# Performance work log

Measured on AMD Instinct MI355X. Metric: run time of the kernel, lower is better.

## Reference

```python
import math
import jax, jax.numpy as jnp
import numpy as np


def _gelu(x):
    return jax.nn.gelu(x, approximate=False)


def _bilinear_sample(feat, gx, gy):
    """grid_sample, mode=bilinear, padding=border, align_corners=True.
    feat: [B,C,H,W]; gx,gy: [B,M] in [-1,1]. Returns [B,M,C]."""
    B, C, H, W = feat.shape
    x = jnp.clip((gx + 1.0) * 0.5 * (W - 1), 0.0, W - 1)
    y = jnp.clip((gy + 1.0) * 0.5 * (H - 1), 0.0, H - 1)
    x0 = jnp.floor(x); y0 = jnp.floor(y)
    wx = (x - x0)[..., None]; wy = (y - y0)[..., None]
    x0i = x0.astype(jnp.int32); y0i = y0.astype(jnp.int32)
    x1i = jnp.minimum(x0i + 1, W - 1); y1i = jnp.minimum(y0i + 1, H - 1)
    ft = jnp.transpose(feat, (0, 2, 3, 1))  # [B,H,W,C]
    gather = jax.vmap(lambda f, yi, xi: f[yi, xi])
    v00 = gather(ft, y0i, x0i); v01 = gather(ft, y0i, x1i)
    v10 = gather(ft, y1i, x0i); v11 = gather(ft, y1i, x1i)
    return (v00 * (1 - wx) * (1 - wy) + v01 * wx * (1 - wy)
            + v10 * (1 - wx) * wy + v11 * wx * wy)


def _layernorm(x, w, b, eps=1e-5):
    m = jnp.mean(x, -1, keepdims=True)
    v = jnp.var(x, -1, keepdims=True)
    return (x - m) / jnp.sqrt(v + eps) * w + b


def _gfb(h, f_next, ph_w, ph_b, gate, w1, b1, w2, b2, ln_w, ln_b):
    g = jax.nn.sigmoid(gate)
    fused = f_next + g * (h @ ph_w + ph_b)
    fused = _gelu(fused @ w1 + b1) @ w2 + b2
    return _layernorm(fused, ln_w, ln_b)


def _forward(img, feat_s8, feat_s16, coarse_flow, query_coords,
             pp_w1, pp_b1, pp_w2, pp_b2, p8_w, p8_b, p16_w, p16_b,
             f1_ph_w, f1_ph_b, f1_gate, f1_w1, f1_b1, f1_w2, f1_b2, f1_ln_w, f1_ln_b,
             f2_ph_w, f2_ph_b, f2_gate, f2_w1, f2_b1, f2_w2, f2_b2, f2_ln_w, f2_ln_b,
             h_w1, h_b1, h_w2, h_b2, h_w3, h_b3):
    B, _, H, W = img.shape
    N = query_coords.shape[1]
    k = 5; half = k // 2
    H8, W8 = coarse_flow.shape[2], coarse_flow.shape[3]
    # normalized grid at query points (x,y)
    gx = 2.0 * query_coords[..., 0] / (W - 1) - 1.0
    gy = 2.0 * query_coords[..., 1] / (H - 1) - 1.0
    coarse_q = _bilinear_sample(coarse_flow, gx, gy)  # [B,N,2]
    coarse_q = coarse_q * jnp.array([W / W8, H / H8], coarse_q.dtype)
    # local k x k RGB patches
    offs = jnp.arange(-half, half + 1, dtype=img.dtype)
    oy, ox = jnp.meshgrid(offs, offs, indexing='ij')
    og = jnp.stack([ox.reshape(-1), oy.reshape(-1)], -1)  # [k*k,2]
    ce = query_coords[:, :, None, :] + og                # [B,N,kk,2]
    pgx = (2.0 * ce[..., 0] / (W - 1) - 1.0).reshape(B, -1)
    pgy = (2.0 * ce[..., 1] / (H - 1) - 1.0).reshape(B, -1)
    patches = _bilinear_sample(img, pgx, pgy).reshape(B, N, k * k * 3)
    f_local = _gelu(patches @ pp_w1 + pp_b1) @ pp_w2 + pp_b2
    f8 = _bilinear_sample(feat_s8, gx, gy) @ p8_w + p8_b
    f16 = _bilinear_sample(feat_s16, gx, gy) @ p16_w + p16_b
    D = f_local.shape[-1]
    h = f_local.reshape(B * N, D)
    h = _gfb(h, f8.reshape(B * N, D), f1_ph_w, f1_ph_b, f1_gate,
             f1_w1, f1_b1, f1_w2, f1_b2, f1_ln_w, f1_ln_b)
    h = _gfb(h, f16.reshape(B * N, D), f2_ph_w, f2_ph_b, f2_gate,
             f2_w1, f2_b1, f2_w2, f2_b2, f2_ln_w, f2_ln_b)
    # relative-in-cell coords + sinusoidal PE (6 bands)
    qx = query_coords[..., 0] / (W / W8)
    qy = query_coords[..., 1] / (H / H8)
    local = jnp.stack([(qx - jnp.round(qx)) * 2.0, (qy - jnp.round(qy)) * 2.0], -1)
    freqs = (2.0 ** jnp.arange(6, dtype=local.dtype)) * math.pi
    xf = local[..., None] * freqs                        # [B,N,2,6]
    enc = jnp.concatenate([jnp.sin(xf), jnp.cos(xf)], -1).reshape(B, N, 24)
    pe = jnp.concatenate([local, enc], -1).reshape(B * N, 26)
    coarse_flat = coarse_q.reshape(B * N, 2)
    mi = jnp.concatenate([h, pe, coarse_flat], -1)       # [B*N, 156]
    delta = _gelu(_gelu(mi @ h_w1 + h_b1) @ h_w2 + h_b2) @ h_w3 + h_b3
    return (coarse_flat + delta).reshape(B, N, 2)


def setup_inputs() -> dict:
    key = jax.random.key(0)
    ks = jax.random.split(key, 40)
    B, H, W = 2, 384, 512
    H8, W8, H16, W16 = 48, 64, 24, 32
    N, D, k = 65536, 128, 5
    pf = 3 * k * k
    def p(i, shape):
        return jax.random.normal(ks[i], shape, jnp.float32) * 0.05
    return {
        'img': jax.random.uniform(ks[0], (B, 3, H, W), jnp.float32),
        'feat_s8': jax.random.normal(ks[1], (B, D, H8, W8), jnp.float32),
        'feat_s16': jax.random.normal(ks[2], (B, D, H16, W16), jnp.float32),
        'coarse_flow': jax.random.normal(ks[3], (B, 2, H8, W8), jnp.float32),
        'query_coords': jax.random.uniform(ks[4], (B, N, 2), jnp.float32)
                        * jnp.array([W - 1.0, H - 1.0], jnp.float32),
        'pp_w1': p(5, (pf, D)), 'pp_b1': p(6, (D,)),
        'pp_w2': p(7, (D, D)), 'pp_b2': p(8, (D,)),
        'p8_w': p(9, (D, D)), 'p8_b': p(10, (D,)),
        'p16_w': p(11, (D, D)), 'p16_b': p(12, (D,)),
        'f1_ph_w': p(13, (D, D)), 'f1_ph_b': p(14, (D,)), 'f1_gate': p(15, (D,)),
        'f1_w1': p(16, (D, 2 * D)), 'f1_b1': p(17, (2 * D,)),
        'f1_w2': p(18, (2 * D, D)), 'f1_b2': p(19, (D,)),
        'f1_ln_w': 1.0 + p(20, (D,)), 'f1_ln_b': p(21, (D,)),
        'f2_ph_w': p(22, (D, D)), 'f2_ph_b': p(23, (D,)), 'f2_gate': p(24, (D,)),
        'f2_w1': p(25, (D, 2 * D)), 'f2_b1': p(26, (2 * D,)),
        'f2_w2': p(27, (2 * D, D)), 'f2_b2': p(28, (D,)),
        'f2_ln_w': 1.0 + p(29, (D,)), 'f2_ln_b': p(30, (D,)),
        'h_w1': p(31, (D + 26 + 2, 128)), 'h_b1': p(32, (128,)),
        'h_w2': p(33, (128, 64)), 'h_b2': p(34, (64,)),
        'h_w3': p(35, (64, 2)), 'h_b3': p(36, (2,)),
    }


def reference(img, feat_s8, feat_s16, coarse_flow, query_coords,
              pp_w1, pp_b1, pp_w2, pp_b2, p8_w, p8_b, p16_w, p16_b,
              f1_ph_w, f1_ph_b, f1_gate, f1_w1, f1_b1, f1_w2, f1_b2, f1_ln_w, f1_ln_b,
              f2_ph_w, f2_ph_b, f2_gate, f2_w1, f2_b1, f2_w2, f2_b2, f2_ln_w, f2_ln_b,
              h_w1, h_b1, h_w2, h_b2, h_w3, h_b3):
    return _forward(img, feat_s8, feat_s16, coarse_flow, query_coords,
                    pp_w1, pp_b1, pp_w2, pp_b2, p8_w, p8_b, p16_w, p16_b,
                    f1_ph_w, f1_ph_b, f1_gate, f1_w1, f1_b1, f1_w2, f1_b2, f1_ln_w, f1_ln_b,
                    f2_ph_w, f2_ph_b, f2_gate, f2_w1, f2_b1, f2_w2, f2_b2, f2_ln_w, f2_ln_b,
                    h_w1, h_b1, h_w2, h_b2, h_w3, h_b3)
```

## Files before the change

kernel.cpp:

```cpp
#include <hip/hip_runtime.h>
#include <math.h>

#define NT 512
#define MB 64
#define MTOT 131072
#define IMG_H 384
#define IMG_W 512
#define H8 48
#define W8 64
#define H16 24
#define W16 32

#define SAB 128
#define SPE 40

typedef _Float16 half8_t __attribute__((ext_vector_type(8)));
typedef _Float16 half4_t __attribute__((ext_vector_type(4)));
typedef float f32x4_t __attribute__((ext_vector_type(4)));
typedef unsigned short u16;

#define SWZ(r, gi) ((gi) ^ ((r) & 7))

#define PW_PP1    0
#define PW_MEGA1  12288
#define PW_S8     77824
#define PW_MEGA2  110592
#define PW_S15    176128
#define PW_HW1    208896
#define PW_HW2    229376
#define PW_END    237568
#define FT8_OFF   PW_END
#define FT8_CNT   (2*H8*W8*128)
#define FT16_OFF  (FT8_OFF + FT8_CNT)
#define FT16_CNT  (2*H16*W16*128)
#define F32_OFF   (FT16_OFF + FT16_CNT)
#define PEG_OFF   (F32_OFF + 2*164480)
#define PEG_CNT   (2048*MB*SPE)
#define CBG_OFF   (PEG_OFF + PEG_CNT)

__device__ __forceinline__ u16 tohalf(float v) {
  return __builtin_bit_cast(u16, (_Float16)v);
}
__device__ __forceinline__ float geluf(float x) {
  float x2 = x * x;
  float t = x * fmaf(x2, 0.0713548162726f, 1.5957691216057308f);
  float e = __expf(-t);
  return x * __builtin_amdgcn_rcpf(1.0f + e);
}

__device__ __forceinline__ float bilin_plane(const float* __restrict__ plane,
                                             int Wd, int Hd, float x, float y) {
  x = fminf(fmaxf(x, 0.f), (float)(Wd - 1));
  y = fminf(fmaxf(y, 0.f), (float)(Hd - 1));
  float x0f = floorf(x), y0f = floorf(y);
  int x0 = (int)x0f, y0 = (int)y0f;
  int x1 = min(x0 + 1, Wd - 1), y1 = min(y0 + 1, Hd - 1);
  float wx = x - x0f, wy = y - y0f;
  const float* r0 = plane + y0 * Wd;
  const float* r1 = plane + y1 * Wd;
  float v00 = r0[x0], v01 = r0[x1], v10 = r1[x0], v11 = r1[x1];
  float top = v00 + wx * (v01 - v00);
  float bot = v10 + wx * (v11 - v10);
  return top + wy * (bot - top);
}

__device__ __forceinline__ void featSample(const u16* __restrict__ ft, int Wd, int Hd,
                                           float x, float y, u16* dstRow,
                                           int i16, int giS) {
  x = fminf(fmaxf(x, 0.f), (float)(Wd - 1));
  y = fminf(fmaxf(y, 0.f), (float)(Hd - 1));
  float x0f = floorf(x), y0f = floorf(y);
  int x0 = (int)x0f, y0 = (int)y0f;
  int x1 = min(x0 + 1, Wd - 1), y1 = min(y0 + 1, Hd - 1);
  _Float16 wx = (_Float16)(x - x0f), wy = (_Float16)(y - y0f);
  half8_t v00 = *reinterpret_cast<const half8_t*>(ft + (y0 * Wd + x0) * 128 + i16 * 8);
  half8_t v01 = *reinterpret_cast<const half8_t*>(ft + (y0 * Wd + x1) * 128 + i16 * 8);
  half8_t v10 = *reinterpret_cast<const half8_t*>(ft + (y1 * Wd + x0) * 128 + i16 * 8);
  half8_t v11 = *reinterpret_cast<const half8_t*>(ft + (y1 * Wd + x1) * 128 + i16 * 8);
  half8_t top = v00 + wx * (v01 - v00);
  half8_t bot = v10 + wx * (v11 - v10);
  half8_t r = top + wy * (bot - top);
  *reinterpret_cast<half8_t*>(dstRow + giS * 8) = r;
}

template <int KT, int SPLITKT, int ACT, int SWB = 1, int NWAVES = 8>
__device__ __forceinline__ void mmv(
    const u16* __restrict__ wpk,
    const u16* aA, const u16* aB, int strB,
    const float* __restrict__ bias,
    u16* ob) {
  const int tid = threadIdx.x;
  const int lane = tid & 63;
  const int w = tid >> 6;
  const int l15 = lane & 15;
  const int g = lane >> 4;
  if (NWAVES == 8 || w < NWAVES) {
    f32x4_t acc[4];
#pragma unroll
    for (int mt = 0; mt < 4; ++mt) acc[mt] = (f32x4_t){0.f, 0.f, 0.f, 0.f};
    __builtin_amdgcn_s_setprio(1);
#pragma unroll
    for (int kt = 0; kt < KT; ++kt) {
      half8_t af[4];
#pragma unroll
      for (int mt = 0; mt < 4; ++mt) {
        const int row = mt * 16 + l15;
        const u16* p;
        if (kt < SPLITKT) {
          p = aA + row * 128 + SWZ(row, kt * 4 + g) * 8;
        } else if (SWB) {
          p = aB + row * 128 + SWZ(row, (kt - SPLITKT) * 4 + g) * 8;
        } else {
          p = aB + row * strB + (kt - SPLITKT) * 32 + g * 8;
        }
        af[mt] = *reinterpret_cast<const half8_t*>(p);
      }
      half8_t bf = *reinterpret_cast<const half8_t*>(wpk + ((w * KT + kt) * 64 + lane) * 8);
#pragma unroll
      for (int mt = 0; mt < 4; ++mt)
        acc[mt] = __builtin_amdgcn_mfma_f32_16x16x32_f16(bf, af[mt], acc[mt], 0, 0, 0);
    }
    __builtin_amdgcn_s_setprio(0);
    const int c0 = (w << 4) + (g << 2);
    f32x4_t bv = *reinterpret_cast<const f32x4_t*>(bias + c0);
#pragma unroll
    for (int mt = 0; mt < 4; ++mt) {
      const int row = (mt << 4) + l15;
      half4_t hv;
#pragma unroll
      for (int r = 0; r < 4; ++r) {
        float v = acc[mt][r] + bv[r];
        if (ACT == 1) v = geluf(v);
        hv[r] = (_Float16)v;
      }
      const int e = row * 128 + (c0 ^ ((row & 7) << 3));
      *reinterpret_cast<half4_t*>(ob + e) = hv;
    }
  }
}

__device__ __forceinline__ void lnorm(const u16* src, u16* dst,
                                      const float* __restrict__ lw,
                                      const float* __restrict__ lb) {
  const int tid = threadIdx.x;
  int q = tid >> 3, s = tid & 7;
  float xs[16];
  float sum = 0.f, sum2 = 0.f;
#pragma unroll
  for (int c8 = 0; c8 < 2; ++c8) {
    const int gi = SWZ(q, 2 * s + c8);
    half8_t v = *reinterpret_cast<const half8_t*>(src + q * 128 + gi * 8);
#pragma unroll
    for (int j = 0; j < 8; ++j) {
      float x = (float)v[j];
      xs[c8 * 8 + j] = x; sum += x; sum2 += x * x;
    }
  }
  sum += __shfl_xor(sum, 1); sum2 += __shfl_xor(sum2, 1);
  sum += __shfl_xor(sum, 2); sum2 += __shfl_xor(sum2, 2);
  sum += __shfl_xor(sum, 4); sum2 += __shfl_xor(sum2, 4);
  float mean = sum * 0.0078125f;
  float var = sum2 * 0.0078125f - mean * mean;
  float rstd = rsqrtf(var + 1e-5f);
#pragma unroll
  for (int c8 = 0; c8 < 2; ++c8) {
    half8_t r;
#pragma unroll
    for (int j = 0; j < 8; ++j) {
      int c = s * 16 + c8 * 8 + j;
      r[j] = (_Float16)((xs[c8 * 8 + j] - mean) * rstd * lw[c] + lb[c]);
    }
    const int gi = SWZ(q, 2 * s + c8);
    *reinterpret_cast<half8_t*>(dst + q * 128 + gi * 8) = r;
  }
}

__global__ void compose1(const float* __restrict__ pp_w2, const float* __restrict__ f1_ph_w,
                         const float* __restrict__ f1_gate, const float* __restrict__ f2_ph_w,
                         const float* __restrict__ f2_gate, const float* __restrict__ p8_b,
                         const float* __restrict__ f1_ph_b, const float* __restrict__ pp_b2,
                         float* __restrict__ Wbot1, float* __restrict__ Wph2s,
                         float* __restrict__ bf1) {
  int idx = blockIdx.x * blockDim.x + threadIdx.x;
  if (idx >= 16384) return;
  int k = idx >> 7, m = idx & 127;
  float sig1 = 1.f / (1.f + expf(-f1_gate[m]));
  float acc = 0.f;
  for (int r = 0; r < 128; ++r) acc += pp_w2[k * 128 + r] * f1_ph_w[r * 128 + m];
  Wbot1[idx] = acc * sig1;
  Wph2s[idx] = f2_ph_w[idx] * (1.f / (1.f + expf(-f2_gate[m])));
  if (k == 0) {
    float b = 0.f;
    for (int r = 0; r < 128; ++r) b += pp_b2[r] * f1_ph_w[r * 128 + m];
    bf1[m] = p8_b[m] + sig1 * f1_ph_b[m] + sig1 * b;
  }
}

__global__ void composeW(const float* __restrict__ p8_w, const float* __restrict__ Wbot1,
                         const float* __restrict__ f1_w1, const float* __restrict__ p16_w,
                         const float* __restrict__ Wph2s, const float* __restrict__ f2_w1,
                         const float* __restrict__ bf1, const float* __restrict__ f1_b1,
                         const float* __restrict__ p16_b, const float* __restrict__ f2_ph_b,
                         const float* __restrict__ f2_gate, const float* __restrict__ f2_b1,
                         float* __restrict__ WAf, float* __restrict__ WBf,
                         float* __restrict__ bA, float* __restrict__ bB) {
  const int n = threadIdx.x;
  const int kb = blockIdx.x;
  if (kb < 256) {
    const float* A = (kb < 128) ? (p8_w + kb * 128) : (Wbot1 + (kb - 128) * 128);
    float acc = 0.f;
    for (int m = 0; m < 128; ++m) acc += A[m] * f1_w1[m * 256 + n];
    WAf[kb * 256 + n] = acc;
  } else if (kb < 512) {
    const int k = kb - 256;
    const float* A = (k < 128) ? (p16_w + k * 128) : (Wph2s + (k - 128) * 128);
    float acc = 0.f;
    for (int m = 0; m < 128; ++m) acc += A[m] * f2_w1[m * 256 + n];
    WBf[k * 256 + n] = acc;
  } else if (kb == 512) {
    float acc = f1_b1[n];
    for (int m = 0; m < 128; ++m) acc += bf1[m] * f1_w1[m * 256 + n];
    bA[n] = acc;
  } else {
    float acc = f2_b1[n];
    for (int m = 0; m < 128; ++m) {
      float sig2 = 1.f / (1.f + expf(-f2_gate[m]));
      acc += (p16_b[m] + sig2 * f2_ph_b[m]) * f2_w1[m * 256 + n];
    }
    bB[n] = acc;
  }
}

struct PackArgs {
  const float *pp_w1, *f1_w2, *f2_w2, *h_w1, *h_w2;
  const float *WAf, *WBf;
  u16* dst;
};

__global__ void pack_weights(PackArgs a) {
  const int KTs[7]   = {3, 8, 8, 8, 8, 5, 4};
  const int Ks[7]    = {75, 256, 256, 256, 256, 156, 128};
  const int bases[8] = {0, 12288, 77824, 110592, 176128, 208896, 229376, 237568};
  int stride = gridDim.x * blockDim.x;
  for (int i = blockIdx.x * blockDim.x + threadIdx.x; i < PW_END; i += stride) {
    int s = 0;
    while (i >= bases[s + 1]) ++s;
    int rem = i - bases[s];
    int e = rem & 511, lane = e >> 3, j = e & 7;
    int ntkt = rem >> 9;
    int kt = ntkt % KTs[s], nt = ntkt / KTs[s];
    int k = kt * 32 + ((lane >> 4) << 3) + j;
    int col = (nt << 4) + (lane & 15);
    float v = 0.f;
    if (k < Ks[s]) {
      switch (s) {
        case 0: v = a.pp_w1[k * 128 + col]; break;
        case 1: v = a.WAf[k * 256 + col]; break;
        case 2: v = a.f1_w2[k * 128 + col]; break;
        case 3: v = a.WBf[k * 256 + col]; break;
        case 4: v = a.f2_w2[k * 128 + col]; break;
        case 5: v = a.h_w1[k * 128 + col]; break;
        case 6: v = a.h_w2[k * 64 + col]; break;
      }
    }
    a.dst[i] = tohalf(v);
  }
}

__global__ void cvt_cl_all(const float* __restrict__ s8, u16* __restrict__ d8,
                           const float* __restrict__ s16, u16* __restrict__ d16) {
  const int tot8 = 2 * 128 * H8 * W8;
  const int tot16 = 2 * 128 * H16 * W16;
  int stride = gridDim.x * blockDim.x;
  for (int i = blockIdx.x * blockDim.x + threadIdx.x; i < tot8 + tot16; i += stride) {
    if (i < tot8) {
      int x = i % W8;
      int t = i / W8;
      int y = t % H8; t /= H8;
      int c = t % 128;
      int b = t / 128;
      d8[((b * H8 + y) * W8 + x) * 128 + c] = tohalf(s8[i]);
    } else {
      int i2 = i - tot8;
      int x = i2 % W16;
      int t = i2 / W16;
      int y = t % H16; t /= H16;
      int c = t % 128;
      int b = t / 128;
      d16[((b * H16 + y) * W16 + x) * 128 + c] = tohalf(s16[i2]);
    }
  }
}

struct KParams {
  const float *img, *coarse_flow, *qc;
  const u16 *wpk, *ft8, *ft16;
  const float *bA, *bB;
  u16* peg;
  float* cbg;
  const float *pp_b1;
  const float *f1_b2, *f1_ln_w, *f1_ln_b;
  const float *f2_b2, *f2_ln_w, *f2_ln_b;
  const float *h_b1, *h_b2, *h_w3, *h_b3;
  float* out;
};

__global__ __launch_bounds__(NT, 2) void ifd_mfma(KParams P) {
  __shared__ __align__(16) u16 smem[4 * MB * SAB];
  u16* ab0 = smem;
  u16* ab1 = smem + MB * SAB;
  u16* tb  = smem + 2 * MB * SAB;
  u16* hb  = smem + 3 * MB * SAB;

  const int tid = threadIdx.x;
  const int m0 = blockIdx.x * MB;
  u16* pegB = P.peg + blockIdx.x * (MB * SPE);
  float* cbgB = P.cbg + blockIdx.x * (MB * 2);

  {
    const int q = tid >> 3, sub = tid & 7;
    const int m = m0 + q, b = m >> 16;
    const float qx = P.qc[2 * m], qy = P.qc[2 * m + 1];
    const float* imgb = P.img + b * 3 * (IMG_H * IMG_W);
#pragma unroll
    for (int j = 0; j < 12; ++j) {
      const int c = sub * 12 + j;
      u16 val = 0;
      if (c < 75) {
        int p = c / 3, ch = c - p * 3;
        int iy = p / 5, ix = p - iy * 5;
        val = tohalf(bilin_plane(imgb + ch * (IMG_H * IMG_W), IMG_W, IMG_H,
                                 qx + (float)(ix - 2), qy + (float)(iy - 2)));
      }
      ab0[q * 128 + (c ^ ((q & 7) << 3))] = val;
    }
  }
  if (tid < 128) {
    const int q = tid >> 1, dim = tid & 1;
    const int m = m0 + q;
    const float qv = P.qc[2 * m + dim];
    const float q8 = qv * 0.125f;
    const float loc = (q8 - rintf(q8)) * 2.f;
    pegB[q * SPE + dim] = tohalf(loc);
    const float th = loc * 3.14159265358979323846f;
    float s = __sinf(th), c = __cosf(th);
    const int base = q * SPE + 2 + dim * 12;
#pragma unroll
    for (int bnd = 0; bnd < 6; ++bnd) {
      pegB[base + bnd] = tohalf(s);
      pegB[base + 6 + bnd] = tohalf(c);
      float s2 = 2.f * s * c;
      c = fmaf(-2.f * s, s, 1.f);
      s = s2;
    }
  } else if (tid < 256) {
    const int t2 = tid - 128, q = t2 >> 1, o = t2 & 1;
    const int m = m0 + q, b = m >> 16;
    const float qx = P.qc[2 * m], qy = P.qc[2 * m + 1];
    const float x8 = qx * (63.f / 511.f), y8 = qy * (47.f / 383.f);
    const float cv = 8.f * bilin_plane(P.coarse_flow + (b * 2 + o) * (H8 * W8),
                                       W8, H8, x8, y8);
    pegB[q * SPE + 26 + o] = tohalf(cv);
    cbgB[q * 2 + o] = cv;
  } else if (tid < 384) {
    const int t2 = tid - 256, q = t2 >> 1, pr = t2 & 1;
    *reinterpret_cast<unsigned int*>(pegB + q * SPE + 28 + 2 * pr) = 0u;
  }
  __syncthreads();

  mmv<3, 3, 1>(P.wpk + PW_PP1, ab0, ab0, 128, P.pp_b1, ab1);
  for (int i = tid; i < MB * 16; i += NT) {
    int q = i >> 4, i16 = i & 15;
    int m = m0 + q, b = m >> 16;
    float x = P.qc[2 * m] * (63.f / 511.f), y = P.qc[2 * m + 1] * (47.f / 383.f);
    featSample(P.ft8 + b * (H8 * W8 * 128), W8, H8, x, y, hb + q * 128,
               i16, SWZ(q, i16));
  }
  __syncthreads();

  mmv<8, 4, 1>(P.wpk + PW_MEGA1, hb, ab1, 128, P.bA, ab0);
  mmv<8, 4, 1>(P.wpk + PW_MEGA1 + 32768, hb, ab1, 128, P.bA + 128, tb);
  __syncthreads();

  mmv<8, 4, 0>(P.wpk + PW_S8, ab0, tb, 128, P.f1_b2, ab1);
  __syncthreads();

  lnorm(ab1, hb, P.f1_ln_w, P.f1_ln_b);
  for (int i = tid; i < MB * 16; i += NT) {
    int q = i >> 4, i16 = i & 15;
    int m = m0 + q, b = m >> 16;
    float x = P.qc[2 * m] * (31.f / 511.f), y = P.qc[2 * m + 1] * (23.f / 383.f);
    featSample(P.ft16 + b * (H16 * W16 * 128), W16, H16, x, y, ab0 + q * 128,
               i16, SWZ(q, i16));
  }
  __syncthreads();

  mmv<8, 4, 1>(P.wpk + PW_MEGA2, ab0, hb, 128, P.bB, ab1);
  mmv<8, 4, 1>(P.wpk + PW_MEGA2 + 32768, ab0, hb, 128, P.bB + 128, tb);
  __syncthreads();

  mmv<8, 4, 0>(P.wpk + PW_S15, ab1, tb, 128, P.f2_b2, ab0);
  __syncthreads();

  lnorm(ab0, hb, P.f2_ln_w, P.f2_ln_b);
  __syncthreads();

  mmv<5, 4, 1, 0>(P.wpk + PW_HW1, hb, pegB, SPE, P.h_b1, ab1);
  __syncthreads();

  mmv<4, 4, 1, 1, 4>(P.wpk + PW_HW2, ab1, ab1, 128, P.h_b2, ab0);
  __syncthreads();

  if (tid < 2 * MB) {
    int q = tid >> 1, o = tid & 1;
    float acc = P.h_b3[o];
    const u16* rp = ab0 + q * 128;
#pragma unroll
    for (int c8 = 0; c8 < 8; ++c8) {
      half8_t v = *reinterpret_cast<const half8_t*>(rp + SWZ(q, c8) * 8);
#pragma unroll
      for (int j = 0; j < 8; ++j) acc += (float)v[j] * P.h_w3[(c8 * 8 + j) * 2 + o];
    }
    P.out[(m0 + q) * 2 + o] = cbgB[q * 2 + o] + acc;
  }
}

extern "C" void kernel_launch(void* const* d_in, const int* in_sizes, int n_in,
                              void* d_out, int out_size, void* d_ws, size_t ws_size,
                              hipStream_t stream) {
  u16* wp = (u16*)d_ws;
  float* fbase = (float*)(wp + F32_OFF);
  float* Wbot1 = fbase;
  float* Wph2s = fbase + 16384;
  float* bf1   = fbase + 32768;
  float* bA    = fbase + 32896;
  float* bB    = fbase + 33152;
  float* WAf   = fbase + 33408;
  float* WBf   = fbase + 98944;
  u16* peg = wp + PEG_OFF;
  float* cbg = (float*)(wp + CBG_OFF);

  const float* pp_w2   = (const float*)d_in[7];
  const float* f1_ph_w = (const float*)d_in[13];
  const float* f1_gate = (const float*)d_in[15];
  const float* f2_ph_w = (const float*)d_in[22];
  const float* f2_gate = (const float*)d_in[24];

  compose1<<<64, 256, 0, stream>>>(pp_w2, f1_ph_w, f1_gate, f2_ph_w, f2_gate,
                                   (const float*)d_in[10], (const float*)d_in[14],
                                   (const float*)d_in[8], Wbot1, Wph2s, bf1);
  composeW<<<514, 256, 0, stream>>>((const float*)d_in[9], Wbot1,
                                    (const float*)d_in[16], (const float*)d_in[11],
                                    Wph2s, (const float*)d_in[25], bf1,
                                    (const float*)d_in[17], (const float*)d_in[12],
                                    (const float*)d_in[23], f2_gate,
                                    (const float*)d_in[26], WAf, WBf, bA, bB);

  PackArgs pa;
  pa.pp_w1 = (const float*)d_in[5];
  pa.f1_w2 = (const float*)d_in[18];
  pa.f2_w2 = (const float*)d_in[27];
  pa.h_w1  = (const float*)d_in[31];
  pa.h_w2  = (const float*)d_in[33];
  pa.WAf = WAf; pa.WBf = WBf;
  pa.dst = wp;
  pack_weights<<<464, 256, 0, stream>>>(pa);
  cvt_cl_all<<<1024, 256, 0, stream>>>((const float*)d_in[1], wp + FT8_OFF,
                                       (const float*)d_in[2], wp + FT16_OFF);

  KParams P;
  P.img = (const float*)d_in[0];
  P.coarse_flow = (const float*)d_in[3];
  P.qc = (const float*)d_in[4];
  P.wpk = wp; P.ft8 = wp + FT8_OFF; P.ft16 = wp + FT16_OFF;
  P.bA = bA; P.bB = bB;
  P.peg = peg; P.cbg = cbg;
  P.pp_b1 = (const float*)d_in[6];
  P.f1_b2 = (const float*)d_in[19];
  P.f1_ln_w = (const float*)d_in[20]; P.f1_ln_b = (const float*)d_in[21];
  P.f2_b2 = (const float*)d_in[28];
  P.f2_ln_w = (const float*)d_in[29]; P.f2_ln_b = (const float*)d_in[30];
  P.h_b1 = (const float*)d_in[32]; P.h_b2 = (const float*)d_in[34];
  P.h_w3 = (const float*)d_in[35]; P.h_b3 = (const float*)d_in[36];
  P.out = (float*)d_out;

  ifd_mfma<<<MTOT / MB, NT, 0, stream>>>(P);
}
```

Before: 192.3 us.

## Reassociate weight-composition matmuls, split-K them, and fold feature conversion into prep

```diff
diff --git a/kernel.cpp b/kernel.cpp
--- a/kernel.cpp
+++ b/kernel.cpp
@@ -34,7 +34,7 @@
 #define FT16_OFF  (FT8_OFF + FT8_CNT)
 #define FT16_CNT  (2*H16*W16*128)
 #define F32_OFF   (FT16_OFF + FT16_CNT)
-#define PEG_OFF   (F32_OFF + 2*164480)
+#define PEG_OFF   (F32_OFF + 2*164608)
 #define PEG_CNT   (2048*MB*SPE)
 #define CBG_OFF   (PEG_OFF + PEG_CNT)
 
@@ -175,65 +175,124 @@
   }
 }
 
-__global__ void compose1(const float* __restrict__ pp_w2, const float* __restrict__ f1_ph_w,
-                         const float* __restrict__ f1_gate, const float* __restrict__ f2_ph_w,
-                         const float* __restrict__ f2_gate, const float* __restrict__ p8_b,
-                         const float* __restrict__ f1_ph_b, const float* __restrict__ pp_b2,
-                         float* __restrict__ Wbot1, float* __restrict__ Wph2s,
-                         float* __restrict__ bf1) {
-  int idx = blockIdx.x * blockDim.x + threadIdx.x;
-  if (idx >= 16384) return;
-  int k = idx >> 7, m = idx & 127;
-  float sig1 = 1.f / (1.f + expf(-f1_gate[m]));
+struct PrepArgs {
+  const float *f1_ph_w, *f1_gate, *f2_ph_w, *f2_gate;
+  const float *p8_w, *p16_w, *f1_w1, *f2_w1;
+  const float *p8_b, *f1_ph_b, *p16_b, *f2_ph_b, *f2_b1;
+  const float *feat8, *feat16;
+  float *T1, *WAtop, *WBtop, *WBbot, *bvec1, *bB;
+  u16 *ft8, *ft16;
+};
+
+__global__ void prepA(PrepArgs a) {
+  const int blk = blockIdx.x;
+  const int tid = threadIdx.x;
+  if (blk < 2056) {
+    const int o = tid >> 2, ks = tid & 3;
+    float acc = 0.f;
+    if (blk < 2048) {
+      const int sec = blk >> 9;
+      const int oid = (blk & 511) * 64 + o;
+      const int r = oid >> 8, n = oid & 255;
+#pragma unroll 8
+      for (int i = 0; i < 32; ++i) {
+        const int m = ks * 32 + i;
+        if (sec == 0) {
+          float sig = __builtin_amdgcn_rcpf(1.f + __expf(-a.f1_gate[m]));
+          acc += sig * a.f1_ph_w[r * 128 + m] * a.f1_w1[m * 256 + n];
+        } else if (sec == 1) {
+          acc += a.p8_w[r * 128 + m] * a.f1_w1[m * 256 + n];
+        } else if (sec == 2) {
+          acc += a.p16_w[r * 128 + m] * a.f2_w1[m * 256 + n];
+        } else {
+          float sig = __builtin_amdgcn_rcpf(1.f + __expf(-a.f2_gate[m]));
+          acc += sig * a.f2_ph_w[r * 128 + m] * a.f2_w1[m * 256 + n];
+        }
+      }
+      acc += __shfl_xor(acc, 1);
+      acc += __shfl_xor(acc, 2);
+      if (ks == 0) {
+        float* dst = (sec == 0) ? a.T1 : (sec == 1) ? a.WAtop
+                     : (sec == 2) ? a.WBtop : a.WBbot;
+        dst[oid] = acc;
+      }
+    } else {
+      const int oid = (blk - 2048) * 64 + o;
+#pragma unroll 8
+      for (int i = 0; i < 32; ++i) {
+        const int m = ks * 32 + i;
+        if (oid < 256) {
+          float sig = __builtin_amdgcn_rcpf(1.f + __expf(-a.f1_gate[m]));
+          acc += (a.p8_b[m] + sig * a.f1_ph_b[m]) * a.f1_w1[m * 256 + oid];
+        } else {
+          float sig = __builtin_amdgcn_rcpf(1.f + __expf(-a.f2_gate[m]));
+          acc += (a.p16_b[m] + sig * a.f2_ph_b[m]) * a.f2_w1[m * 256 + (oid - 256)];
+        }
+      }
+      acc += __shfl_xor(acc, 1);
+      acc += __shfl_xor(acc, 2);
+      if (ks == 0) {
+        if (oid < 256) a.bvec1[oid] = acc;
+        else a.bB[oid - 256] = a.f2_b1[oid - 256] + acc;
+      }
+    }
+  } else {
+    const int tot8 = 2 * 128 * H8 * W8;
+    const int i = (blk - 2056) * 256 + tid;
+    if (i < tot8) {
+      int x = i % W8;
+      int t = i / W8;
+      int y = t % H8; t /= H8;
+      int c = t % 128;
+      int b = t / 128;
+      a.ft8[((b * H8 + y) * W8 + x) * 128 + c] = tohalf(a.feat8[i]);
+    } else {
+      int i2 = i - tot8;
+      int x = i2 % W16;
+      int t = i2 / W16;
+      int y = t % H16; t /= H16;
+      int c = t % 128;
+      int b = t / 128;
+      a.ft16[((b * H16 + y) * W16 + x) * 128 + c] = tohalf(a.feat16[i2]);
+    }
+  }
+}
+
+__global__ void prepB(const float* __restrict__ pp_w2, const float* __restrict__ T1,
+                      const float* __restrict__ pp_b2, const float* __restrict__ f1_b1,
+                      const float* __restrict__ bvec1,
+                      float* __restrict__ WAbot, float* __restrict__ bA) {
+  const int blk = blockIdx.x;
+  const int tid = threadIdx.x;
+  const int o = tid >> 2, ks = tid & 3;
   float acc = 0.f;
-  for (int r = 0; r < 128; ++r) acc += pp_w2[k * 128 + r] * f1_ph_w[r * 128 + m];
-  Wbot1[idx] = acc * sig1;
-  Wph2s[idx] = f2_ph_w[idx] * (1.f / (1.f + expf(-f2_gate[m])));
-  if (k == 0) {
-    float b = 0.f;
-    for (int r = 0; r < 128; ++r) b += pp_b2[r] * f1_ph_w[r * 128 + m];
-    bf1[m] = p8_b[m] + sig1 * f1_ph_b[m] + sig1 * b;
-  }
-}
-
-__global__ void composeW(const float* __restrict__ p8_w, const float* __restrict__ Wbot1,
-                         const float* __restrict__ f1_w1, const float* __restrict__ p16_w,
-                         const float* __restrict__ Wph2s, const float* __restrict__ f2_w1,
-                         const float* __restrict__ bf1, const float* __restrict__ f1_b1,
-                         const float* __restrict__ p16_b, const float* __restrict__ f2_ph_b,
-                         const float* __restrict__ f2_gate, const float* __restrict__ f2_b1,
-                         float* __restrict__ WAf, float* __restrict__ WBf,
-                         float* __restrict__ bA, float* __restrict__ bB) {
-  const int n = threadIdx.x;
-  const int kb = blockIdx.x;
-  if (kb < 256) {
-    const float* A = (kb < 128) ? (p8_w + kb * 128) : (Wbot1 + (kb - 128) * 128);
-    float acc = 0.f;
-    for (int m = 0; m < 128; ++m) acc += A[m] * f1_w1[m * 256 + n];
-    WAf[kb * 256 + n] = acc;
-  } else if (kb < 512) {
-    const int k = kb - 256;
-    const float* A = (k < 128) ? (p16_w + k * 128) : (Wph2s + (k - 128) * 128);
-    float acc = 0.f;
-    for (int m = 0; m < 128; ++m) acc += A[m] * f2_w1[m * 256 + n];
-    WBf[k * 256 + n] = acc;
-  } else if (kb == 512) {
-    float acc = f1_b1[n];
-    for (int m = 0; m < 128; ++m) acc += bf1[m] * f1_w1[m * 256 + n];
-    bA[n] = acc;
+  if (blk < 512) {
+    const int oid = blk * 64 + o;
+    const int k = oid >> 8, n = oid & 255;
+#pragma unroll 8
+    for (int i = 0; i < 32; ++i) {
+      const int r = ks * 32 + i;
+      acc += pp_w2[k * 128 + r] * T1[r * 256 + n];
+    }
+    acc += __shfl_xor(acc, 1);
+    acc += __shfl_xor(acc, 2);
+    if (ks == 0) WAbot[oid] = acc;
   } else {
-    float acc = f2_b1[n];
-    for (int m = 0; m < 128; ++m) {
-      float sig2 = 1.f / (1.f + expf(-f2_gate[m]));
-      acc += (p16_b[m] + sig2 * f2_ph_b[m]) * f2_w1[m * 256 + n];
-    }
-    bB[n] = acc;
+    const int n = (blk - 512) * 64 + o;
+#pragma unroll 8
+    for (int i = 0; i < 32; ++i) {
+      const int r = ks * 32 + i;
+      acc += pp_b2[r] * T1[r * 256 + n];
+    }
+    acc += __shfl_xor(acc, 1);
+    acc += __shfl_xor(acc, 2);
+    if (ks == 0) bA[n] = f1_b1[n] + bvec1[n] + acc;
   }
 }
 
 struct PackArgs {
   const float *pp_w1, *f1_w2, *f2_w2, *h_w1, *h_w2;
-  const float *WAf, *WBf;
+  const float *WAtop, *WAbot, *WBtop, *WBbot;
   u16* dst;
 };
 
@@ -255,40 +314,17 @@
     if (k < Ks[s]) {
       switch (s) {
         case 0: v = a.pp_w1[k * 128 + col]; break;
-        case 1: v = a.WAf[k * 256 + col]; break;
+        case 1: v = (k < 128) ? a.WAtop[k * 256 + col]
+                              : a.WAbot[(k - 128) * 256 + col]; break;
         case 2: v = a.f1_w2[k * 128 + col]; break;
-        case 3: v = a.WBf[k * 256 + col]; break;
+        case 3: v = (k < 128) ? a.WBtop[k * 256 + col]
+                              : a.WBbot[(k - 128) * 256 + col]; break;
         case 4: v = a.f2_w2[k * 128 + col]; break;
         case 5: v = a.h_w1[k * 128 + col]; break;
         case 6: v = a.h_w2[k * 64 + col]; break;
       }
     }
     a.dst[i] = tohalf(v);
-  }
-}
-
-__global__ void cvt_cl_all(const float* __restrict__ s8, u16* __restrict__ d8,
-                           const float* __restrict__ s16, u16* __restrict__ d16) {
-  const int tot8 = 2 * 128 * H8 * W8;
-  const int tot16 = 2 * 128 * H16 * W16;
-  int stride = gridDim.x * blockDim.x;
-  for (int i = blockIdx.x * blockDim.x + threadIdx.x; i < tot8 + tot16; i += stride) {
-    if (i < tot8) {
-      int x = i % W8;
-      int t = i / W8;
-      int y = t % H8; t /= H8;
-      int c = t % 128;
-      int b = t / 128;
-      d8[((b * H8 + y) * W8 + x) * 128 + c] = tohalf(s8[i]);
-    } else {
-      int i2 = i - tot8;
-      int x = i2 % W16;
-      int t = i2 / W16;
-      int y = t % H16; t /= H16;
-      int c = t % 128;
-      int b = t / 128;
-      d16[((b * H16 + y) * W16 + x) * 128 + c] = tohalf(s16[i2]);
-    }
   }
 }
 
@@ -430,31 +466,40 @@
                               hipStream_t stream) {
   u16* wp = (u16*)d_ws;
   float* fbase = (float*)(wp + F32_OFF);
-  float* Wbot1 = fbase;
-  float* Wph2s = fbase + 16384;
-  float* bf1   = fbase + 32768;
-  float* bA    = fbase + 32896;
-  float* bB    = fbase + 33152;
-  float* WAf   = fbase + 33408;
-  float* WBf   = fbase + 98944;
+  float* T1    = fbase;
+  float* WAtop = fbase + 32768;
+  float* WAbot = fbase + 65536;
+  float* WBtop = fbase + 98304;
+  float* WBbot = fbase + 131072;
+  float* bvec1 = fbase + 163840;
+  float* bA    = fbase + 164096;
+  float* bB    = fbase + 164352;
   u16* peg = wp + PEG_OFF;
   float* cbg = (float*)(wp + CBG_OFF);
 
-  const float* pp_w2   = (const float*)d_in[7];
-  const float* f1_ph_w = (const float*)d_in[13];
-  const float* f1_gate = (const float*)d_in[15];
-  const float* f2_ph_w = (const float*)d_in[22];
-  const float* f2_gate = (const float*)d_in[24];
-
-  compose1<<<64, 256, 0, stream>>>(pp_w2, f1_ph_w, f1_gate, f2_ph_w, f2_gate,
-                                   (const float*)d_in[10], (const float*)d_in[14],
-                                   (const float*)d_in[8], Wbot1, Wph2s, bf1);
-  composeW<<<514, 256, 0, stream>>>((const float*)d_in[9], Wbot1,
-                                    (const float*)d_in[16], (const float*)d_in[11],
-                                    Wph2s, (const float*)d_in[25], bf1,
-                                    (const float*)d_in[17], (const float*)d_in[12],
-                                    (const float*)d_in[23], f2_gate,
-                                    (const float*)d_in[26], WAf, WBf, bA, bB);
+  PrepArgs pra;
+  pra.f1_ph_w = (const float*)d_in[13];
+  pra.f1_gate = (const float*)d_in[15];
+  pra.f2_ph_w = (const float*)d_in[22];
+  pra.f2_gate = (const float*)d_in[24];
+  pra.p8_w = (const float*)d_in[9];
+  pra.p16_w = (const float*)d_in[11];
+  pra.f1_w1 = (const float*)d_in[16];
+  pra.f2_w1 = (const float*)d_in[25];
+  pra.p8_b = (const float*)d_in[10];
+  pra.f1_ph_b = (const float*)d_in[14];
+  pra.p16_b = (const float*)d_in[12];
+  pra.f2_ph_b = (const float*)d_in[23];
+  pra.f2_b1 = (const float*)d_in[26];
+  pra.feat8 = (const float*)d_in[1];
+  pra.feat16 = (const float*)d_in[2];
+  pra.T1 = T1; pra.WAtop = WAtop; pra.WBtop = WBtop; pra.WBbot = WBbot;
+  pra.bvec1 = bvec1; pra.bB = bB;
+  pra.ft8 = wp + FT8_OFF; pra.ft16 = wp + FT16_OFF;
+  prepA<<<2056 + 3840, 256, 0, stream>>>(pra);
+
+  prepB<<<516, 256, 0, stream>>>((const float*)d_in[7], T1, (const float*)d_in[8],
+                                 (const float*)d_in[17], bvec1, WAbot, bA);
 
   PackArgs pa;
   pa.pp_w1 = (const float*)d_in[5];
@@ -462,11 +507,9 @@
   pa.f2_w2 = (const float*)d_in[27];
   pa.h_w1  = (const float*)d_in[31];
   pa.h_w2  = (const float*)d_in[33];
-  pa.WAf = WAf; pa.WBf = WBf;
+  pa.WAtop = WAtop; pa.WAbot = WAbot; pa.WBtop = WBtop; pa.WBbot = WBbot;
   pa.dst = wp;
   pack_weights<<<464, 256, 0, stream>>>(pa);
-  cvt_cl_all<<<1024, 256, 0, stream>>>((const float*)d_in[1], wp + FT8_OFF,
-                                       (const float*)d_in[2], wp + FT16_OFF);
 
   KParams P;
   P.img = (const float*)d_in[0];
```

New measurement: 196.5 us. 1.02x slower.
